# Optimization experiments

Hardware: AMD Instinct MI355X
Metric: run time of the kernel (lower is better)

The kernel has to match this reference:

```python
import jax, jax.numpy as jnp
import numpy as np


def setup_inputs() -> dict:
    key0 = jax.random.key(0)
    kq, kk, kv, kl = jax.random.split(key0, 4)
    B, L, V, D = 2, 512, 64, 128
    N_CLUSTERS = 8
    return {
        "query": jax.random.normal(kq, (B, L, V, D), dtype=jnp.float32),
        "key": jax.random.normal(kk, (B, L, V, D), dtype=jnp.float32),
        "value": jax.random.normal(kv, (B, L, V, D), dtype=jnp.float32),
        "label_arr": jax.random.randint(kl, (B, L), 0, N_CLUSTERS, dtype=jnp.int64)
        if jax.config.jax_enable_x64
        else jax.random.randint(kl, (B, L), 0, N_CLUSTERS, dtype=jnp.int32),
    }


def reference(query, key, value, label_arr):
    # query/key/value: (b, l, v, d); label_arr: (b, l)
    b, l, v, d = query.shape
    scale = 1.0 / (d ** 0.5)  # self.scale defaults to 1/sqrt(d_model)

    # sum of key over the v (cluster-member) dimension -> (b, l, d)
    sum_tot_vec = key.sum(axis=2)

    # scores[b,i,k,j] = query[b,i,k,:] . sum_tot_vec[b,j,:]
    scores = jnp.einsum("bikd,bjd->bikj", query, sum_tot_vec)

    # label-based mask: positions attend only within the same cluster label
    label_mask = label_arr[:, :, None] == label_arr[:, None, :]  # (b, l, l)
    scores = jnp.where(label_mask[:, :, None, :], scores, -jnp.inf)

    # masked softmax over the last (j) axis; every row has >=1 valid entry (self)
    A = jax.nn.softmax(scale * scores, axis=-1)

    # V[b,i,k,d] = sum_j A[b,i,k,j] * value[b,j,k,d]
    out = jnp.einsum("bikj,bjkd->bikd", A, value)
    return out
```

## Files before the change

### kernel.cpp

```cpp
#include <hip/hip_runtime.h>
#include <math.h>

#define B_ 2
#define L_ 512
#define V_ 64
#define D_ 128
#define NC_ 8
#define SCALE 0.08838834764831845f

#define THREADS 128
#define IT 64
#define JT 8
#define MAXIT (L_ / IT)

__device__ __forceinline__ float dpp8_sum(float x) {
  x += __int_as_float(__builtin_amdgcn_mov_dpp(__float_as_int(x), 0xB1, 0xF, 0xF, true));
  x += __int_as_float(__builtin_amdgcn_mov_dpp(__float_as_int(x), 0x4E, 0xF, 0xF, true));
  x += __int_as_float(__builtin_amdgcn_mov_dpp(__float_as_int(x), 0x141, 0xF, 0xF, true));
  return x;
}

__global__ __launch_bounds__(L_) void cluster_index_kernel(
    const int* __restrict__ label, int* __restrict__ counts, int* __restrict__ jlist) {
  int b = blockIdx.x;
  int tid = threadIdx.x;
  __shared__ int lab[L_];
  lab[tid] = label[b * L_ + tid];
  if (tid < NC_) counts[b * NC_ + tid] = 0;
  __syncthreads();
  int my = lab[tid];
  int rank = 0, cnt = 0;
  for (int j = 0; j < L_; ++j) {
    int e = (lab[j] == my) ? 1 : 0;
    cnt += e;
    if (j < tid) rank += e;
  }
  jlist[(b * NC_ + my) * L_ + rank] = tid;
  if (rank == 0) counts[b * NC_ + my] = cnt;
}

__global__ __launch_bounds__(256) void sumkey_kernel(
    const float* __restrict__ key, float* __restrict__ S) {
  int idx = blockIdx.x * 256 + threadIdx.x;
  int d = idx & (D_ - 1);
  int bj = idx >> 7;
  const float* kp = key + (size_t)bj * V_ * D_ + d;
  float s = 0.f;
#pragma unroll 8
  for (int v = 0; v < V_; ++v) s += kp[v * D_];
  S[idx] = s;
}

__global__ __launch_bounds__(THREADS, 2) void clustered_attn_kernel(
    const float* __restrict__ q, const float* __restrict__ value,
    const float* __restrict__ S, const int* __restrict__ counts,
    const int* __restrict__ jlist, float* __restrict__ out) {
  int bid = blockIdx.x;
  int k = bid & (V_ - 1);
  int c = (bid >> 6) & (NC_ - 1);
  int b = (bid >> 9) & (B_ - 1);
  int itile = bid >> 10;
  int n = counts[b * NC_ + c];
  int it0 = itile * IT;
  if (it0 >= n) return;

  int tid = threadIdx.x;
  int dh = tid & 7;
  int sl = tid >> 3;

  __shared__ int jl[L_];
  __shared__ float S_t[JT][D_];
  __shared__ float V_t[JT][D_];

  for (int j = tid; j < n; j += THREADS) jl[j] = jlist[(b * NC_ + c) * L_ + j];
  __syncthreads();

  bool act[4];
  float4 q4[4][4];
#pragma unroll
  for (int r = 0; r < 4; ++r) {
    int row = it0 + sl + 16 * r;
    act[r] = row < n;
    int i = jl[act[r] ? row : it0];
    const float* qrow = q + (size_t)((b * L_ + i) * V_ + k) * D_;
#pragma unroll
    for (int t = 0; t < 4; ++t)
      q4[r][t] = *(const float4*)(qrow + (dh + 8 * t) * 4);
  }

  float4 acc4[4][4];
#pragma unroll
  for (int r = 0; r < 4; ++r)
#pragma unroll
    for (int t = 0; t < 4; ++t) acc4[r][t] = make_float4(0.f, 0.f, 0.f, 0.f);
  float m[4], l[4];
#pragma unroll
  for (int r = 0; r < 4; ++r) { m[r] = -INFINITY; l[r] = 0.f; }

  const float4* S_t4 = (const float4*)&S_t[0][0];
  const float4* V_t4 = (const float4*)&V_t[0][0];

  for (int jt0 = 0; jt0 < n; jt0 += JT) {
    int jn = min(JT, n - jt0);
    __syncthreads();
#pragma unroll
    for (int rep = 0; rep < 2; ++rep) {
      int idx = tid + rep * THREADS;
      int jj = idx >> 5;
      int d4 = idx & 31;
      int j = jl[jt0 + min(jj, jn - 1)];
      size_t rowbase = (size_t)(b * L_ + j);
      ((float4*)&S_t[0][0])[idx] = *(const float4*)(S + rowbase * D_ + d4 * 4);
      ((float4*)&V_t[0][0])[idx] =
          *(const float4*)(value + (rowbase * V_ + k) * D_ + d4 * 4);
    }
    __syncthreads();

    float s[4][JT];
#pragma unroll
    for (int r = 0; r < 4; ++r)
#pragma unroll
      for (int jj = 0; jj < JT; ++jj) s[r][jj] = 0.f;
#pragma unroll
    for (int t = 0; t < 4; ++t) {
#pragma unroll
      for (int jj = 0; jj < JT; ++jj) {
        float4 sv = S_t4[jj * 32 + dh + 8 * t];
#pragma unroll
        for (int r = 0; r < 4; ++r) {
          float4 qv = q4[r][t];
          s[r][jj] = fmaf(qv.x, sv.x,
                     fmaf(qv.y, sv.y,
                     fmaf(qv.z, sv.z, fmaf(qv.w, sv.w, s[r][jj]))));
        }
      }
    }
#pragma unroll
    for (int r = 0; r < 4; ++r)
#pragma unroll
      for (int jj = 0; jj < JT; ++jj)
        s[r][jj] = dpp8_sum(s[r][jj]) * SCALE;

#pragma unroll
    for (int r = 0; r < 4; ++r) {
      float mnew = m[r];
#pragma unroll
      for (int jj = 0; jj < JT; ++jj)
        if (jj < jn) mnew = fmaxf(mnew, s[r][jj]);
      float f = __expf(m[r] - mnew);
      m[r] = mnew;
#pragma unroll
      for (int t = 0; t < 4; ++t) {
        acc4[r][t].x *= f; acc4[r][t].y *= f;
        acc4[r][t].z *= f; acc4[r][t].w *= f;
      }
      float sum = 0.f;
#pragma unroll
      for (int jj = 0; jj < JT; ++jj) {
        float p = (jj < jn) ? __expf(s[r][jj] - mnew) : 0.f;
        s[r][jj] = p;
        sum += p;
      }
      l[r] = l[r] * f + sum;
    }

#pragma unroll
    for (int t = 0; t < 4; ++t) {
#pragma unroll
      for (int jj = 0; jj < JT; ++jj) {
        float4 vv = V_t4[jj * 32 + dh + 8 * t];
#pragma unroll
        for (int r = 0; r < 4; ++r) {
          float p = s[r][jj];
          acc4[r][t].x = fmaf(p, vv.x, acc4[r][t].x);
          acc4[r][t].y = fmaf(p, vv.y, acc4[r][t].y);
          acc4[r][t].z = fmaf(p, vv.z, acc4[r][t].z);
          acc4[r][t].w = fmaf(p, vv.w, acc4[r][t].w);
        }
      }
    }
  }

#pragma unroll
  for (int r = 0; r < 4; ++r) {
    if (act[r]) {
      int i = jl[it0 + sl + 16 * r];
      float inv = 1.0f / l[r];
      float* op = out + (size_t)((b * L_ + i) * V_ + k) * D_;
#pragma unroll
      for (int t = 0; t < 4; ++t) {
        float4 o;
        o.x = acc4[r][t].x * inv;
        o.y = acc4[r][t].y * inv;
        o.z = acc4[r][t].z * inv;
        o.w = acc4[r][t].w * inv;
        *(float4*)(op + (dh + 8 * t) * 4) = o;
      }
    }
  }
}

extern "C" void kernel_launch(void* const* d_in, const int* in_sizes, int n_in,
                              void* d_out, int out_size, void* d_ws, size_t ws_size,
                              hipStream_t stream) {
  const float* q = (const float*)d_in[0];
  const float* key = (const float*)d_in[1];
  const float* value = (const float*)d_in[2];
  const int* label = (const int*)d_in[3];
  float* out = (float*)d_out;

  int* counts = (int*)d_ws;
  int* jlist = (int*)((char*)d_ws + 256);
  float* S = (float*)((char*)d_ws + 256 + B_ * NC_ * L_ * sizeof(int));

  cluster_index_kernel<<<B_, L_, 0, stream>>>(label, counts, jlist);
  sumkey_kernel<<<(B_ * L_ * D_) / 256, 256, 0, stream>>>(key, S);
  clustered_attn_kernel<<<B_ * NC_ * V_ * MAXIT, THREADS, 0, stream>>>(
      q, value, S, counts, jlist, out);
}
```

Before: 248.6 us.

## Split attention into MFMA QK-softmax and PV kernels with bf16x2 split precision

Replaces the fused scalar-FMA flash-style kernel with two MFMA kernels for clusters of at most 128 members. The first computes scores and a full softmax using bf16 hi/lo split operands, and writes probabilities as bf16 to a workspace. The second transposes value into LDS as hi/lo bf16 and multiplies it by those probabilities. The old kernel remains as a fallback for large clusters or a small workspace. This trades ALU-bound FP32 FMA work for matrix cores, but adds a round trip of the probability matrix through global memory and some loss of precision because probabilities are stored as single bf16.

```diff
diff --git a/kernel.cpp b/kernel.cpp
--- a/kernel.cpp
+++ b/kernel.cpp
@@ -6,18 +6,25 @@
 #define V_ 64
 #define D_ 128
 #define NC_ 8
+#define NMAX 128
+#define NPAD 8
 #define SCALE 0.08838834764831845f
 
-#define THREADS 128
-#define IT 64
-#define JT 8
-#define MAXIT (L_ / IT)
-
-__device__ __forceinline__ float dpp8_sum(float x) {
-  x += __int_as_float(__builtin_amdgcn_mov_dpp(__float_as_int(x), 0xB1, 0xF, 0xF, true));
-  x += __int_as_float(__builtin_amdgcn_mov_dpp(__float_as_int(x), 0x4E, 0xF, 0xF, true));
-  x += __int_as_float(__builtin_amdgcn_mov_dpp(__float_as_int(x), 0x141, 0xF, 0xF, true));
-  return x;
+#define FB_THREADS 128
+#define FB_IT 64
+#define FB_JT 8
+#define MAXIT (L_ / FB_IT)
+
+typedef short s16x8 __attribute__((ext_vector_type(8)));
+typedef float f32x4 __attribute__((ext_vector_type(4)));
+
+__device__ __forceinline__ unsigned short f2bf(float x) {
+  unsigned int u = __float_as_uint(x);
+  u += 0x7FFFu + ((u >> 16) & 1u);
+  return (unsigned short)(u >> 16);
+}
+__device__ __forceinline__ float bf2f(unsigned short h) {
+  return __uint_as_float((unsigned int)h << 16);
 }
 
 __global__ __launch_bounds__(L_) void cluster_index_kernel(
@@ -40,28 +47,242 @@
 }
 
 __global__ __launch_bounds__(256) void sumkey_kernel(
-    const float* __restrict__ key, float* __restrict__ S) {
+    const float* __restrict__ key, float* __restrict__ S,
+    unsigned short* __restrict__ Sh, unsigned short* __restrict__ Sl, int do16) {
   int idx = blockIdx.x * 256 + threadIdx.x;
-  int d = idx & (D_ - 1);
-  int bj = idx >> 7;
-  const float* kp = key + (size_t)bj * V_ * D_ + d;
-  float s = 0.f;
+  int d4 = idx & 31;
+  int bj = idx >> 5;
+  const float4* kp = (const float4*)(key + (size_t)bj * V_ * D_) + d4;
+  float4 s = make_float4(0.f, 0.f, 0.f, 0.f);
 #pragma unroll 8
-  for (int v = 0; v < V_; ++v) s += kp[v * D_];
-  S[idx] = s;
-}
-
-__global__ __launch_bounds__(THREADS, 2) void clustered_attn_kernel(
+  for (int v = 0; v < V_; ++v) {
+    float4 x = kp[v * 32];
+    s.x += x.x; s.y += x.y; s.z += x.z; s.w += x.w;
+  }
+  *((float4*)S + idx) = s;
+  if (do16) {
+    unsigned short h0 = f2bf(s.x), h1 = f2bf(s.y), h2 = f2bf(s.z), h3 = f2bf(s.w);
+    *((ushort4*)Sh + idx) = make_ushort4(h0, h1, h2, h3);
+    *((ushort4*)Sl + idx) = make_ushort4(
+        f2bf(s.x - bf2f(h0)), f2bf(s.y - bf2f(h1)),
+        f2bf(s.z - bf2f(h2)), f2bf(s.w - bf2f(h3)));
+  }
+}
+
+__global__ void pbase_kernel(const int* __restrict__ counts,
+                             int* __restrict__ pbase, int* __restrict__ pflag,
+                             long long cap, int force) {
+  if (blockIdx.x == 0 && threadIdx.x == 0) {
+    long long acc = 0;
+    for (int bc = 0; bc < B_ * NC_; ++bc) {
+      int n = counts[bc];
+      int np = (n + 31) & ~31;
+      long long sz = (n > 0 && n <= NMAX) ? (long long)V_ * n * np : 0;
+      int bad = (force || n == 0 || n > NMAX || acc + sz > cap) ? 1 : 0;
+      pflag[bc] = bad;
+      pbase[bc] = (int)acc;
+      if (!bad) acc += sz;
+    }
+  }
+}
+
+__global__ __launch_bounds__(256) void qk_softmax_kernel(
+    const float* __restrict__ q, const unsigned short* __restrict__ Sh,
+    const unsigned short* __restrict__ Sl,
+    const int* __restrict__ counts, const int* __restrict__ jlist,
+    const int* __restrict__ pbase, const int* __restrict__ pflag,
+    unsigned short* __restrict__ P) {
+  int bid = blockIdx.x;
+  int ii = bid & (NMAX - 1);
+  int c = (bid >> 7) & (NC_ - 1);
+  int b = bid >> 10;
+  int bc = b * NC_ + c;
+  int n = counts[bc];
+  if (n > NMAX || ii >= n || pflag[bc]) return;
+  int np = (n + 31) & ~31;
+  int nt = np >> 4;
+  int base = pbase[bc];
+
+  int tid = threadIdx.x;
+  int w = tid >> 6, l = tid & 63, lr = l & 15, lg = l >> 4;
+
+  __shared__ int jl[NMAX];
+  for (int j = tid; j < np; j += 256) jl[j] = jlist[bc * L_ + min(j, n - 1)];
+  __syncthreads();
+
+  int i = jlist[bc * L_ + ii];
+
+  const float* qb = q + ((size_t)(b * L_ + i) * V_ + 16 * w + lr) * D_ + lg * 8;
+  s16x8 Ah[4], Al[4];
+#pragma unroll
+  for (int kk = 0; kk < 4; ++kk) {
+    float4 x0 = *(const float4*)(qb + kk * 32);
+    float4 x1 = *(const float4*)(qb + kk * 32 + 4);
+    float xs[8] = {x0.x, x0.y, x0.z, x0.w, x1.x, x1.y, x1.z, x1.w};
+#pragma unroll
+    for (int e = 0; e < 8; ++e) {
+      unsigned short h = f2bf(xs[e]);
+      Ah[kk][e] = (short)h;
+      Al[kk][e] = (short)f2bf(xs[e] - bf2f(h));
+    }
+  }
+
+  f32x4 cacc[8];
+#pragma unroll
+  for (int jt = 0; jt < 8; ++jt) {
+    if (jt < nt) {
+      int jrow = jl[jt * 16 + lr];
+      const unsigned short* sbh = Sh + (size_t)(b * L_ + jrow) * D_ + lg * 8;
+      const unsigned short* sbl = Sl + (size_t)(b * L_ + jrow) * D_ + lg * 8;
+      f32x4 acc = {0.f, 0.f, 0.f, 0.f};
+#pragma unroll
+      for (int kk = 0; kk < 4; ++kk) {
+        s16x8 bh = *(const s16x8*)(sbh + kk * 32);
+        s16x8 bl = *(const s16x8*)(sbl + kk * 32);
+        acc = __builtin_amdgcn_mfma_f32_16x16x32_bf16(Ah[kk], bh, acc, 0, 0, 0);
+        acc = __builtin_amdgcn_mfma_f32_16x16x32_bf16(Al[kk], bh, acc, 0, 0, 0);
+        acc = __builtin_amdgcn_mfma_f32_16x16x32_bf16(Ah[kk], bl, acc, 0, 0, 0);
+      }
+      cacc[jt] = acc;
+    }
+  }
+
+#pragma unroll
+  for (int reg = 0; reg < 4; ++reg) {
+    float sv[8];
+    float mx = -3.0e38f;
+#pragma unroll
+    for (int jt = 0; jt < 8; ++jt) {
+      if (jt < nt) {
+        float x = ((jt * 16 + lr) < n) ? cacc[jt][reg] * SCALE : -3.0e38f;
+        sv[jt] = x;
+        mx = fmaxf(mx, x);
+      }
+    }
+    mx = fmaxf(mx, __shfl_xor(mx, 1));
+    mx = fmaxf(mx, __shfl_xor(mx, 2));
+    mx = fmaxf(mx, __shfl_xor(mx, 4));
+    mx = fmaxf(mx, __shfl_xor(mx, 8));
+    float sum = 0.f;
+#pragma unroll
+    for (int jt = 0; jt < 8; ++jt) {
+      if (jt < nt) {
+        float p = __expf(sv[jt] - mx);
+        p = ((jt * 16 + lr) < n) ? p : 0.f;
+        sv[jt] = p;
+        sum += p;
+      }
+    }
+    sum += __shfl_xor(sum, 1);
+    sum += __shfl_xor(sum, 2);
+    sum += __shfl_xor(sum, 4);
+    sum += __shfl_xor(sum, 8);
+    float inv = 1.0f / sum;
+    int krow = 16 * w + lg * 4 + reg;
+    int rb = base + (krow * n + ii) * np;
+#pragma unroll
+    for (int jt = 0; jt < 8; ++jt)
+      if (jt < nt) P[rb + jt * 16 + lr] = f2bf(sv[jt] * inv);
+  }
+}
+
+__global__ __launch_bounds__(256) void pv_kernel(
+    const float* __restrict__ vg, const int* __restrict__ counts,
+    const int* __restrict__ jlist, const int* __restrict__ pbase,
+    const int* __restrict__ pflag, const unsigned short* __restrict__ P,
+    float* __restrict__ out) {
+  int bid = blockIdx.x;
+  int k = bid & (V_ - 1);
+  int c = (bid >> 6) & (NC_ - 1);
+  int b = bid >> 9;
+  int bc = b * NC_ + c;
+  int n = counts[bc];
+  if (n == 0 || n > NMAX || pflag[bc]) return;
+  int np = (n + 31) & ~31;
+  int ktn = np >> 5;
+  int stride = np + NPAD;
+  int base = pbase[bc];
+  int mt = (n + 15) >> 4;
+
+  int tid = threadIdx.x;
+  int w = tid >> 6, l = tid & 63, lr = l & 15, lg = l >> 4;
+
+  __shared__ int jl[NMAX];
+  __shared__ __align__(16) unsigned short Vth[64 * (NMAX + NPAD)];
+  __shared__ __align__(16) unsigned short Vtl[64 * (NMAX + NPAD)];
+
+  for (int j = tid; j < np; j += 256) jl[j] = jlist[bc * L_ + min(j, n - 1)];
+  __syncthreads();
+
+  for (int dh = 0; dh < 2; ++dh) {
+    if (dh) __syncthreads();
+    int d4 = tid & 15;
+    for (int j0 = 0; j0 < np; j0 += 16) {
+      int jj = j0 + (tid >> 4);
+      float4 x = make_float4(0.f, 0.f, 0.f, 0.f);
+      if (jj < n)
+        x = *(const float4*)(vg + ((size_t)(b * L_ + jl[jj]) * V_ + k) * D_
+                             + dh * 64 + d4 * 4);
+      float xs[4] = {x.x, x.y, x.z, x.w};
+#pragma unroll
+      for (int e = 0; e < 4; ++e) {
+        unsigned short h = f2bf(xs[e]);
+        Vth[(d4 * 4 + e) * stride + jj] = h;
+        Vtl[(d4 * 4 + e) * stride + jj] = f2bf(xs[e] - bf2f(h));
+      }
+    }
+    __syncthreads();
+
+    s16x8 bh[4], bl[4];
+#pragma unroll
+    for (int kt = 0; kt < 4; ++kt) {
+      if (kt < ktn) {
+        int off = (w * 16 + lr) * stride + kt * 32 + lg * 8;
+        bh[kt] = *(const s16x8*)(Vth + off);
+        bl[kt] = *(const s16x8*)(Vtl + off);
+      }
+    }
+
+#pragma unroll
+    for (int mi = 0; mi < 8; ++mi) {
+      if (mi < mt) {
+        int irow = min(mi * 16 + lr, n - 1);
+        const unsigned short* pa = P + base + ((size_t)k * n + irow) * np + lg * 8;
+        f32x4 acc = {0.f, 0.f, 0.f, 0.f};
+#pragma unroll
+        for (int kt = 0; kt < 4; ++kt) {
+          if (kt < ktn) {
+            s16x8 af = *(const s16x8*)(pa + kt * 32);
+            acc = __builtin_amdgcn_mfma_f32_16x16x32_bf16(af, bh[kt], acc, 0, 0, 0);
+            acc = __builtin_amdgcn_mfma_f32_16x16x32_bf16(af, bl[kt], acc, 0, 0, 0);
+          }
+        }
+#pragma unroll
+        for (int reg = 0; reg < 4; ++reg) {
+          int i = mi * 16 + lg * 4 + reg;
+          if (i < n)
+            out[((size_t)(b * L_ + jl[i]) * V_ + k) * D_ + dh * 64 + w * 16 + lr]
+                = acc[reg];
+        }
+      }
+    }
+  }
+}
+
+__global__ __launch_bounds__(FB_THREADS, 2) void clustered_attn_kernel(
     const float* __restrict__ q, const float* __restrict__ value,
     const float* __restrict__ S, const int* __restrict__ counts,
-    const int* __restrict__ jlist, float* __restrict__ out) {
+    const int* __restrict__ jlist, const int* __restrict__ pflag, int force,
+    float* __restrict__ out) {
   int bid = blockIdx.x;
   int k = bid & (V_ - 1);
   int c = (bid >> 6) & (NC_ - 1);
   int b = (bid >> 9) & (B_ - 1);
   int itile = bid >> 10;
-  int n = counts[b * NC_ + c];
-  int it0 = itile * IT;
+  int bc = b * NC_ + c;
+  int n = counts[bc];
+  if (!(force || n > NMAX || pflag[bc])) return;
+  int it0 = itile * FB_IT;
   if (it0 >= n) return;
 
   int tid = threadIdx.x;
@@ -69,10 +290,10 @@
   int sl = tid >> 3;
 
   __shared__ int jl[L_];
-  __shared__ float S_t[JT][D_];
-  __shared__ float V_t[JT][D_];
-
-  for (int j = tid; j < n; j += THREADS) jl[j] = jlist[(b * NC_ + c) * L_ + j];
+  __shared__ float S_t[FB_JT][D_];
+  __shared__ float V_t[FB_JT][D_];
+
+  for (int j = tid; j < n; j += FB_THREADS) jl[j] = jlist[bc * L_ + j];
   __syncthreads();
 
   bool act[4];
@@ -84,8 +305,7 @@
     int i = jl[act[r] ? row : it0];
     const float* qrow = q + (size_t)((b * L_ + i) * V_ + k) * D_;
 #pragma unroll
-    for (int t = 0; t < 4; ++t)
-      q4[r][t] = *(const float4*)(qrow + (dh + 8 * t) * 4);
+    for (int t = 0; t < 4; ++t) q4[r][t] = *(const float4*)(qrow + (dh + 8 * t) * 4);
   }
 
   float4 acc4[4][4];
@@ -93,19 +313,19 @@
   for (int r = 0; r < 4; ++r)
 #pragma unroll
     for (int t = 0; t < 4; ++t) acc4[r][t] = make_float4(0.f, 0.f, 0.f, 0.f);
-  float m[4], l[4];
-#pragma unroll
-  for (int r = 0; r < 4; ++r) { m[r] = -INFINITY; l[r] = 0.f; }
+  float m[4], lden[4];
+#pragma unroll
+  for (int r = 0; r < 4; ++r) { m[r] = -INFINITY; lden[r] = 0.f; }
 
   const float4* S_t4 = (const float4*)&S_t[0][0];
   const float4* V_t4 = (const float4*)&V_t[0][0];
 
-  for (int jt0 = 0; jt0 < n; jt0 += JT) {
-    int jn = min(JT, n - jt0);
+  for (int jt0 = 0; jt0 < n; jt0 += FB_JT) {
+    int jn = min(FB_JT, n - jt0);
     __syncthreads();
 #pragma unroll
     for (int rep = 0; rep < 2; ++rep) {
-      int idx = tid + rep * THREADS;
+      int idx = tid + rep * FB_THREADS;
       int jj = idx >> 5;
       int d4 = idx & 31;
       int j = jl[jt0 + min(jj, jn - 1)];
@@ -116,36 +336,38 @@
     }
     __syncthreads();
 
-    float s[4][JT];
+    float s[4][FB_JT];
 #pragma unroll
     for (int r = 0; r < 4; ++r)
 #pragma unroll
-      for (int jj = 0; jj < JT; ++jj) s[r][jj] = 0.f;
+      for (int jj = 0; jj < FB_JT; ++jj) s[r][jj] = 0.f;
 #pragma unroll
     for (int t = 0; t < 4; ++t) {
 #pragma unroll
-      for (int jj = 0; jj < JT; ++jj) {
+      for (int jj = 0; jj < FB_JT; ++jj) {
         float4 sv = S_t4[jj * 32 + dh + 8 * t];
 #pragma unroll
         for (int r = 0; r < 4; ++r) {
           float4 qv = q4[r][t];
           s[r][jj] = fmaf(qv.x, sv.x,
-                     fmaf(qv.y, sv.y,
-                     fmaf(qv.z, sv.z, fmaf(qv.w, sv.w, s[r][jj]))));
+                     fmaf(qv.y, sv.y, fmaf(qv.z, sv.z, fmaf(qv.w, sv.w, s[r][jj]))));
         }
       }
     }
 #pragma unroll
     for (int r = 0; r < 4; ++r)
 #pragma unroll
-      for (int jj = 0; jj < JT; ++jj)
-        s[r][jj] = dpp8_sum(s[r][jj]) * SCALE;
-
+      for (int jj = 0; jj < FB_JT; ++jj) {
+        float v = s[r][jj] + __shfl_xor(s[r][jj], 1);
+        v += __shfl_xor(v, 2);
+        v += __shfl_xor(v, 4);
+        s[r][jj] = v * SCALE;
+      }
 #pragma unroll
     for (int r = 0; r < 4; ++r) {
       float mnew = m[r];
 #pragma unroll
-      for (int jj = 0; jj < JT; ++jj)
+      for (int jj = 0; jj < FB_JT; ++jj)
         if (jj < jn) mnew = fmaxf(mnew, s[r][jj]);
       float f = __expf(m[r] - mnew);
       m[r] = mnew;
@@ -156,18 +378,17 @@
       }
       float sum = 0.f;
 #pragma unroll
-      for (int jj = 0; jj < JT; ++jj) {
+      for (int jj = 0; jj < FB_JT; ++jj) {
         float p = (jj < jn) ? __expf(s[r][jj] - mnew) : 0.f;
         s[r][jj] = p;
         sum += p;
       }
-      l[r] = l[r] * f + sum;
-    }
-
+      lden[r] = lden[r] * f + sum;
+    }
 #pragma unroll
     for (int t = 0; t < 4; ++t) {
 #pragma unroll
-      for (int jj = 0; jj < JT; ++jj) {
+      for (int jj = 0; jj < FB_JT; ++jj) {
         float4 vv = V_t4[jj * 32 + dh + 8 * t];
 #pragma unroll
         for (int r = 0; r < 4; ++r) {
@@ -185,7 +406,7 @@
   for (int r = 0; r < 4; ++r) {
     if (act[r]) {
       int i = jl[it0 + sl + 16 * r];
-      float inv = 1.0f / l[r];
+      float inv = 1.0f / lden[r];
       float* op = out + (size_t)((b * L_ + i) * V_ + k) * D_;
 #pragma unroll
       for (int t = 0; t < 4; ++t) {
@@ -209,12 +430,29 @@
   const int* label = (const int*)d_in[3];
   float* out = (float*)d_out;
 
-  int* counts = (int*)d_ws;
-  int* jlist = (int*)((char*)d_ws + 256);
-  float* S = (float*)((char*)d_ws + 256 + B_ * NC_ * L_ * sizeof(int));
+  char* w8 = (char*)d_ws;
+  int* counts = (int*)(w8 + 0);
+  int* pbase = (int*)(w8 + 64);
+  int* pflag = (int*)(w8 + 128);
+  int* jlist = (int*)(w8 + 256);
+  float* S = (float*)(w8 + 33280);
+  unsigned short* Sh = (unsigned short*)(w8 + 557568);
+  unsigned short* Sl = (unsigned short*)(w8 + 819712);
+  unsigned short* P = (unsigned short*)(w8 + 1081856);
+
+  long long cap = 0;
+  if (ws_size > (size_t)1081856) cap = (long long)((ws_size - 1081856) / 2);
+  int mfma_ok = (cap >= (1LL << 20)) ? 1 : 0;
 
   cluster_index_kernel<<<B_, L_, 0, stream>>>(label, counts, jlist);
-  sumkey_kernel<<<(B_ * L_ * D_) / 256, 256, 0, stream>>>(key, S);
-  clustered_attn_kernel<<<B_ * NC_ * V_ * MAXIT, THREADS, 0, stream>>>(
-      q, value, S, counts, jlist, out);
-}
+  sumkey_kernel<<<(B_ * L_ * D_ / 4) / 256, 256, 0, stream>>>(key, S, Sh, Sl, mfma_ok);
+  pbase_kernel<<<1, 64, 0, stream>>>(counts, pbase, pflag, cap, mfma_ok ? 0 : 1);
+  if (mfma_ok) {
+    qk_softmax_kernel<<<B_ * NC_ * NMAX, 256, 0, stream>>>(
+        q, Sh, Sl, counts, jlist, pbase, pflag, P);
+    pv_kernel<<<B_ * NC_ * V_, 256, 0, stream>>>(
+        value, counts, jlist, pbase, pflag, P, out);
+  }
+  clustered_attn_kernel<<<B_ * NC_ * V_ * MAXIT, FB_THREADS, 0, stream>>>(
+      q, value, S, counts, jlist, pflag, mfma_ok ? 0 : 1, out);
+}
```

Result: faster. 208.7 us (-16.1%).
